# Kernel tuning notes

Hardware: AMD Instinct MI355X
Metric: run time of the kernel (lower is better)

The kernel has to match this reference:

```python
import jax, jax.numpy as jnp
import numpy as np

N0, N1, N2 = 100000, 50000, 20000
D = 128
E0, E1 = 600000, 300000


def _sage_rel(x_src, x_dst, src, dst, Ws, Wn, b, n_dst):
    """DGL SAGEConv(mean): fc_self(x_dst) + fc_neigh(mean of in-neighbors) + b."""
    msg = x_src[src]                                              # [E, D] gather
    ssum = jax.ops.segment_sum(msg, dst, num_segments=n_dst)      # [n_dst, D]
    deg = jax.ops.segment_sum(jnp.ones(dst.shape, x_src.dtype), dst, num_segments=n_dst)
    h_neigh = ssum / jnp.maximum(deg, 1.0)[:, None]               # zero-degree -> 0
    return x_dst @ Ws + h_neigh @ Wn + b


def setup_inputs() -> dict:
    key = jax.random.key(0)
    ks = jax.random.split(key, 24)
    p = 0.05
    inp = {
        "x": jax.random.normal(ks[0], (N0, D), jnp.float32),
        "e0_src_r0": jax.random.randint(ks[1], (E0,), 0, N0),
        "e0_dst_r0": jax.random.randint(ks[2], (E0,), 0, N1),
        "e0_src_r1": jax.random.randint(ks[3], (E0,), 0, N0),
        "e0_dst_r1": jax.random.randint(ks[4], (E0,), 0, N1),
        "e1_src_r0": jax.random.randint(ks[5], (E1,), 0, N1),
        "e1_dst_r0": jax.random.randint(ks[6], (E1,), 0, N2),
        "e1_src_r1": jax.random.randint(ks[7], (E1,), 0, N1),
        "e1_dst_r1": jax.random.randint(ks[8], (E1,), 0, N2),
    }
    names = ["Ws1_r0", "Wn1_r0", "Ws1_r1", "Wn1_r1", "Ws2_r0", "Wn2_r0", "Ws2_r1", "Wn2_r1"]
    for i, n in enumerate(names):
        inp[n] = jax.random.normal(ks[9 + i], (D, D), jnp.float32) * p
    for i, n in enumerate(["b1_r0", "b1_r1", "b2_r0", "b2_r1"]):
        inp[n] = jax.random.normal(ks[17 + i], (D,), jnp.float32) * p
    return inp


def reference(x, e0_src_r0, e0_dst_r0, e0_src_r1, e0_dst_r1,
              e1_src_r0, e1_dst_r0, e1_src_r1, e1_dst_r1,
              Ws1_r0, Wn1_r0, b1_r0, Ws1_r1, Wn1_r1, b1_r1,
              Ws2_r0, Wn2_r0, b2_r0, Ws2_r1, Wn2_r1, b2_r1):
    # Layer 1: HeteroGraphConv sum over relations, then ReLU
    x_dst1 = x[:N1]
    h1 = (_sage_rel(x, x_dst1, e0_src_r0, e0_dst_r0, Ws1_r0, Wn1_r0, b1_r0, N1)
          + _sage_rel(x, x_dst1, e0_src_r1, e0_dst_r1, Ws1_r1, Wn1_r1, b1_r1, N1))
    h1 = jax.nn.relu(h1)
    # Layer 2
    h1_dst = h1[:N2]
    h2 = (_sage_rel(h1, h1_dst, e1_src_r0, e1_dst_r0, Ws2_r0, Wn2_r0, b2_r0, N2)
          + _sage_rel(h1, h1_dst, e1_src_r1, e1_dst_r1, Ws2_r1, Wn2_r1, b2_r1, N2))
    return h2
```

## Files before the change

kernel.cpp:

```cpp
#include <hip/hip_runtime.h>
#include <hip/hip_bf16.h>
#include <hip/hip_fp8.h>

#define N0 100000
#define N1 50000
#define N2 20000
#define DD 128
#define E0 600000
#define E1 300000

#define NSEG_TOT (2 * N1 + 2 * N2)
#define ETOT     (2 * E0 + 2 * E1)

#define SEG_SHIFT 9
#define NBK  ((NSEG_TOT + 511) / 512)
#define CH   2048
#define NCH  ((ETOT + CH - 1) / CH)
#define PADCAP 8192

#define CAST_BLOCKS 6250
#define PREP_BLOCKS 48
#define PROLOGUE_BLOCKS (CAST_BLOCKS + PREP_BLOCKS + NCH)

typedef __attribute__((ext_vector_type(8))) short short8;
typedef __attribute__((ext_vector_type(4))) float floatx4;
typedef __attribute__((ext_vector_type(2))) float floatx2;

__device__ __forceinline__ void st2bf(__hip_bfloat16* p, float a, float b) {
    __hip_bfloat162 v;
    v.x = __float2bfloat16(a);
    v.y = __float2bfloat16(b);
    *(__hip_bfloat162*)p = v;
}
__device__ __forceinline__ short bf16bits(float v) {
    __hip_bfloat16 b = __float2bfloat16(v);
    return *(short*)&b;
}
__device__ __forceinline__ float bf2f(unsigned short u) {
    return __uint_as_float(((unsigned int)u) << 16);
}
__device__ __forceinline__ float4 ld4bf(const __hip_bfloat16* p) {
    ushort4 u = *(const ushort4*)p;
    return make_float4(bf2f(u.x), bf2f(u.y), bf2f(u.z), bf2f(u.w));
}
__device__ __forceinline__ void st4bf(__hip_bfloat16* p, float4 v) {
    short vs[4];
    vs[0] = bf16bits(v.x); vs[1] = bf16bits(v.y);
    vs[2] = bf16bits(v.z); vs[3] = bf16bits(v.w);
    *(int2*)p = *(int2*)vs;
}

__device__ __forceinline__ unsigned f8enc4(float x, float y, float z, float w) {
    int v = 0;
    v = __builtin_amdgcn_cvt_pk_fp8_f32(x, y, v, false);
    v = __builtin_amdgcn_cvt_pk_fp8_f32(z, w, v, true);
    return (unsigned)v;
}
__device__ __forceinline__ void f8acc8m(unsigned lo, unsigned hi, float m, float* acc) {
    floatx2 p0 = __builtin_amdgcn_cvt_pk_f32_fp8((int)lo, false);
    floatx2 p1 = __builtin_amdgcn_cvt_pk_f32_fp8((int)lo, true);
    floatx2 p2 = __builtin_amdgcn_cvt_pk_f32_fp8((int)hi, false);
    floatx2 p3 = __builtin_amdgcn_cvt_pk_f32_fp8((int)hi, true);
    acc[0] = fmaf(m, p0[0], acc[0]); acc[1] = fmaf(m, p0[1], acc[1]);
    acc[2] = fmaf(m, p1[0], acc[2]); acc[3] = fmaf(m, p1[1], acc[3]);
    acc[4] = fmaf(m, p2[0], acc[4]); acc[5] = fmaf(m, p2[1], acc[5]);
    acc[6] = fmaf(m, p3[0], acc[6]); acc[7] = fmaf(m, p3[1], acc[7]);
}

__device__ __forceinline__ int scan256(int s, int* sh, int t) {
    sh[t] = s;
    __syncthreads();
    for (int off = 1; off < 256; off <<= 1) {
        int tmp = (t >= off) ? sh[t - off] : 0;
        __syncthreads();
        sh[t] += tmp;
        __syncthreads();
    }
    return sh[t];
}

__device__ __forceinline__ int2 edge_seg_src(int e,
    const int* s0, const int* d0, const int* s1, const int* d1,
    const int* s2, const int* d2, const int* s3, const int* d3)
{
    if (e < E0)               return make_int2(s0[e],            d0[e]);
    if (e < 2 * E0)           return make_int2(s1[e - E0],       N1 + d1[e - E0]);
    if (e < 2 * E0 + E1)      return make_int2(s2[e - 2 * E0],   2 * N1 + d2[e - 2 * E0]);
    int ee = e - 2 * E0 - E1;
    return make_int2(s3[ee], 2 * N1 + N2 + d3[ee]);
}

__global__ __launch_bounds__(256) void prologue_kernel(
    const float* __restrict__ x, __hip_bfloat16* __restrict__ xb,
    unsigned char* __restrict__ xf8,
    const int* __restrict__ s0a, const int* __restrict__ d0a,
    const int* __restrict__ s0b, const int* __restrict__ d0b,
    const int* __restrict__ s1a, const int* __restrict__ d1a,
    const int* __restrict__ s1b, const int* __restrict__ d1b,
    int* __restrict__ cntmat, int* __restrict__ ofsmat,
    unsigned* __restrict__ chunkbuf,
    const float* __restrict__ Ws1a, const float* __restrict__ Ws1b,
    const float* __restrict__ Wn1a, const float* __restrict__ Wn1b,
    const float* __restrict__ Ws2a, const float* __restrict__ Ws2b,
    const float* __restrict__ Wn2a, const float* __restrict__ Wn2b,
    short* __restrict__ wfrag1, short* __restrict__ wfrag2)
{
    __shared__ int hist[512];
    __shared__ int ofs[512];
    __shared__ int sh[256];
    __shared__ unsigned rec[CH];
    const int bid = blockIdx.x;
    const int t = threadIdx.x;

    if (bid < CAST_BLOCKS) {
        int i = bid * 256 + t;
        const float4* xp = (const float4*)x + (size_t)i * 2;
        float4 a = xp[0], b = xp[1];
        __hip_bfloat16* pb = xb + (size_t)i * 8;
        st2bf(pb + 0, a.x, a.y); st2bf(pb + 2, a.z, a.w);
        st2bf(pb + 4, b.x, b.y); st2bf(pb + 6, b.z, b.w);
        uint2 w8;
        w8.x = f8enc4(a.x, a.y, a.z, a.w);
        w8.y = f8enc4(b.x, b.y, b.z, b.w);
        *(uint2*)(xf8 + (size_t)i * 8) = w8;
    } else if (bid < CAST_BLOCKS + PREP_BLOCKS) {
        int p = (bid - CAST_BLOCKS) * 256 + t;
        int layer = p >= 6144;
        int q = p - layer * 6144;
        int lane = q & 63;
        int mt = (q >> 6) & 7;
        int kc = q >> 9;
        int n = mt * 16 + (lane & 15);
        int k0 = kc * 32 + ((lane >> 4) << 3);
        const float* Wsa = layer ? Ws2a : Ws1a;
        const float* Wsb = layer ? Ws2b : Ws1b;
        const float* Wna = layer ? Wn2a : Wn1a;
        const float* Wnb = layer ? Wn2b : Wn1b;
        short* wf = layer ? wfrag2 : wfrag1;
        short vals[8];
#pragma unroll
        for (int j = 0; j < 8; j++) {
            int k = k0 + j;
            float w;
            if (k < 128)      w = Wsa[k * DD + n] + Wsb[k * DD + n];
            else if (k < 256) w = Wna[(k - 128) * DD + n];
            else              w = Wnb[(k - 256) * DD + n];
            vals[j] = bf16bits(w);
        }
        *(short8*)(wf + (size_t)q * 8) = *(short8*)vals;
    } else {
        const int chunk = bid - CAST_BLOCKS - PREP_BLOCKS;
        const int ebase = chunk * CH;
        const int ecount = (ETOT - ebase < CH) ? (ETOT - ebase) : CH;

        hist[t] = 0; hist[t + 256] = 0;
        __syncthreads();

        int2 myrec[CH / 256];
#pragma unroll
        for (int it = 0; it < CH / 256; it++) {
            int e = ebase + it * 256 + t;
            int2 r = make_int2(0, -1);
            if (e < ETOT) {
                r = edge_seg_src(e, s0a, d0a, s0b, d0b, s1a, d1a, s1b, d1b);
                atomicAdd(&hist[r.y >> SEG_SHIFT], 1);
            }
            myrec[it] = r;
        }
        __syncthreads();

        const int l0 = 2 * t, l1 = 2 * t + 1;
        int c0 = hist[l0], c1 = hist[l1];
        int s = c0 + c1;
        int incl = scan256(s, sh, t);
        int ex = incl - s;
        ofs[l0] = ex;
        ofs[l1] = ex + c0;
        __syncthreads();

        for (int g = t; g < NBK; g += 256) {
            cntmat[(size_t)g * NCH + chunk] = hist[g];
            ofsmat[(size_t)g * NCH + chunk] = ofs[g];
        }
        __syncthreads();

#pragma unroll
        for (int it = 0; it < CH / 256; it++) {
            int2 r = myrec[it];
            if (r.y >= 0) {
                int rk = atomicAdd(&ofs[r.y >> SEG_SHIFT], 1);
                rec[rk] = (unsigned)r.x | ((unsigned)(r.y & 511) << 17);
            }
        }
        __syncthreads();

        for (int i = t; i < ecount; i += 256)
            chunkbuf[ebase + i] = rec[i];
    }
}

__global__ __launch_bounds__(256) void csr_finalize_kernel(
    const unsigned* __restrict__ chunkbuf,
    const int* __restrict__ cntmat, const int* __restrict__ ofsmat,
    int* __restrict__ row_beg, int* __restrict__ row_cnt,
    int* __restrict__ eidx)
{
    __shared__ int sh[256];
    __shared__ int preL[NCH];
    __shared__ int lenL[NCH];
    __shared__ int cnt[512];
    __shared__ int excl[512];
    __shared__ unsigned rec[PADCAP];
    const int t = threadIdx.x;
    const int g = blockIdx.x;
    const int l0 = 2 * t, l1 = 2 * t + 1;

    int v[4]; int s = 0;
#pragma unroll
    for (int i = 0; i < 4; i++) {
        int idx = t * 4 + i;
        v[i] = (idx < NCH) ? cntmat[(size_t)g * NCH + idx] : 0;
        s += v[i];
    }
    int incl = scan256(s, sh, t);
    int ex = incl - s;
#pragma unroll
    for (int i = 0; i < 4; i++) {
        int idx = t * 4 + i;
        if (idx < NCH) { preL[idx] = ex; lenL[idx] = v[i]; }
        ex += v[i];
    }
    int Eloc = sh[255];
    if (Eloc > PADCAP) Eloc = PADCAP;
    cnt[l0] = 0; cnt[l1] = 0;
    __syncthreads();

    for (int c = t; c < NCH; c += 256) {
        int len = lenL[c];
        int dst = preL[c];
        int off = ofsmat[(size_t)g * NCH + c];
        const unsigned* src = chunkbuf + (size_t)c * CH + off;
        for (int i = 0; i < len; i++) rec[dst + i] = src[i];
    }
    __syncthreads();

    for (int i = t; i < Eloc; i += 256)
        atomicAdd(&cnt[rec[i] >> 17], 1);
    __syncthreads();

    int c0 = cnt[l0], c1 = cnt[l1];
    int ssum = c0 + c1;
    int inc2 = scan256(ssum, sh, t);
    int ex2 = inc2 - ssum;
    excl[l0] = ex2;
    excl[l1] = ex2 + c0;
    __syncthreads();

    const int segbase = g << SEG_SHIFT;
    const int base = g * PADCAP;
    int nloc = NSEG_TOT - segbase;
    if (nloc > 512) nloc = 512;
    for (int l = t; l < nloc; l += 256) {
        row_beg[segbase + l] = base + excl[l];
        row_cnt[segbase + l] = cnt[l];
    }
    __syncthreads();
    cnt[l0] = 0; cnt[l1] = 0;
    __syncthreads();

    for (int i = t; i < Eloc; i += 256) {
        unsigned r = rec[i];
        int l = r >> 17;
        int pos = atomicAdd(&cnt[l], 1);
        eidx[base + excl[l] + pos] = (int)(r & 0x1FFFF);
    }
}

__global__ __launch_bounds__(256) void aggregate_fp8_kernel(
    const unsigned char* __restrict__ xf8,
    const int* __restrict__ row_beg, const int* __restrict__ row_cnt,
    const int* __restrict__ eidx,
    __hip_bfloat16* __restrict__ hn,
    int nseg)
{
    int wid = (blockIdx.x * 256 + threadIdx.x) >> 6;
    const int lane = threadIdx.x & 63;
    if (wid >= nseg) return;
    wid = __builtin_amdgcn_readfirstlane(wid);

    const int beg = row_beg[wid];
    const int cnt = row_cnt[wid];
    const int end = beg + cnt;
    const int q = lane >> 4;
    const int l16 = lane & 15;

    float acc[8];
#pragma unroll
    for (int j = 0; j < 8; j++) acc[j] = 0.f;

    for (int kb = beg; kb < end; kb += 16) {
        int nrows = end - kb;
        if (nrows > 16) nrows = 16;
        int myidx = eidx[kb + (l16 < nrows ? l16 : nrows - 1)];
        uint2 vv[4];
        float mm[4];
#pragma unroll
        for (int j = 0; j < 4; j++) {
            int r = q + 4 * j;
            int sl = r < nrows ? r : nrows - 1;
            int ri = __shfl(myidx, sl);
            vv[j] = *(const uint2*)(xf8 + (size_t)ri * DD + l16 * 8);
            mm[j] = (r < nrows) ? 1.f : 0.f;
        }
#pragma unroll
        for (int j = 0; j < 4; j++)
            f8acc8m(vv[j].x, vv[j].y, mm[j], acc);
    }

#pragma unroll
    for (int j = 0; j < 8; j++) {
        acc[j] += __shfl_xor(acc[j], 16);
        acc[j] += __shfl_xor(acc[j], 32);
    }

    if (lane < 16) {
        const float inv = 1.f / (float)(cnt > 1 ? cnt : 1);
        short vs[8];
#pragma unroll
        for (int j = 0; j < 8; j++) vs[j] = bf16bits(acc[j] * inv);
        *(int4*)(hn + (size_t)wid * DD + l16 * 8) = *(int4*)vs;
    }
}

__global__ __launch_bounds__(256) void aggregate_kernel(
    const __hip_bfloat16* __restrict__ xb,
    const int* __restrict__ row_beg, const int* __restrict__ row_cnt,
    const int* __restrict__ eidx,
    __hip_bfloat16* __restrict__ hn,
    int nseg)
{
    int wid = (blockIdx.x * 256 + threadIdx.x) >> 6;
    const int lane = threadIdx.x & 63;
    if (wid >= nseg) return;
    wid = __builtin_amdgcn_readfirstlane(wid);

    const int beg = row_beg[wid];
    const int cnt = row_cnt[wid];
    const int end = beg + cnt;
    const int half = lane >> 5;
    const int l32 = lane & 31;

    float4 s = make_float4(0.f, 0.f, 0.f, 0.f);
    for (int kb = beg; kb < end; kb += 16) {
        int nrows = end - kb;
        if (nrows > 16) nrows = 16;
        int myidx = eidx[kb + (l32 < nrows ? l32 : nrows - 1)];
        ushort4 vv[8];
        float mm[8];
#pragma unroll
        for (int j = 0; j < 8; j++) {
            int r = half + 2 * j;
            int sl = r < nrows ? r : nrows - 1;
            int ri = __shfl(myidx, sl);
            vv[j] = *(const ushort4*)(xb + (long)ri * DD + l32 * 4);
            mm[j] = (r < nrows) ? 1.f : 0.f;
        }
#pragma unroll
        for (int j = 0; j < 8; j++) {
            s.x = fmaf(mm[j], bf2f(vv[j].x), s.x);
            s.y = fmaf(mm[j], bf2f(vv[j].y), s.y);
            s.z = fmaf(mm[j], bf2f(vv[j].z), s.z);
            s.w = fmaf(mm[j], bf2f(vv[j].w), s.w);
        }
    }

    s.x += __shfl_xor(s.x, 32);
    s.y += __shfl_xor(s.y, 32);
    s.z += __shfl_xor(s.z, 32);
    s.w += __shfl_xor(s.w, 32);

    if (!half) {
        const float inv = 1.f / (float)(cnt > 1 ? cnt : 1);
        float4 m = make_float4(s.x * inv, s.y * inv, s.z * inv, s.w * inv);
        st4bf(hn + (long)wid * DD + l32 * 4, m);
    }
}

template <bool RELU, typename TOUT>
__global__ __launch_bounds__(256) void mfma_combine_kernel(
    const __hip_bfloat16* __restrict__ xself,
    const __hip_bfloat16* __restrict__ hn,
    const short* __restrict__ wfrag,
    const float* __restrict__ b0, const float* __restrict__ b1,
    TOUT* __restrict__ out, int M)
{
    const int t = threadIdx.x;
    const int wave = t >> 6;
    const int lane = t & 63;
    const int nsub = lane & 15;
    const int quad = lane >> 4;
    const int base = blockIdx.x * 128 + wave * 32;

    const int node0 = base + nsub;
    const int node1 = base + 16 + nsub;
    const long n0c = node0 < M ? node0 : M - 1;
    const long n1c = node1 < M ? node1 : M - 1;

    floatx4 acc[2][8];
#pragma unroll
    for (int nt = 0; nt < 2; nt++)
#pragma unroll
        for (int mt = 0; mt < 8; mt++) acc[nt][mt] = (floatx4){0.f, 0.f, 0.f, 0.f};

    for (int kc = 0; kc < 12; kc++) {
        const __hip_bfloat16* src;
        long r0, r1;
        int koff;
        if (kc < 4)      { src = xself; koff = kc * 32;       r0 = n0c;     r1 = n1c; }
        else if (kc < 8) { src = hn;    koff = (kc - 4) * 32; r0 = n0c;     r1 = n1c; }
        else             { src = hn;    koff = (kc - 8) * 32; r0 = M + n0c; r1 = M + n1c; }

        short8 bf0 = *(const short8*)(src + r0 * DD + koff + quad * 8);
        short8 bf1 = *(const short8*)(src + r1 * DD + koff + quad * 8);
        const short* wbase = wfrag + ((size_t)(kc * 8) * 64 + lane) * 8;
#pragma unroll
        for (int mt = 0; mt < 8; mt++) {
            short8 af = *(const short8*)(wbase + (size_t)mt * 64 * 8);
            acc[0][mt] = __builtin_amdgcn_mfma_f32_16x16x32_bf16(af, bf0, acc[0][mt], 0, 0, 0);
            acc[1][mt] = __builtin_amdgcn_mfma_f32_16x16x32_bf16(af, bf1, acc[1][mt], 0, 0, 0);
        }
    }

#pragma unroll
    for (int nt = 0; nt < 2; nt++) {
        int node = (nt == 0) ? node0 : node1;
        if (node >= M) continue;
#pragma unroll
        for (int mt = 0; mt < 8; mt++) {
            int c0 = mt * 16 + quad * 4;
            float4 bb0 = *(const float4*)(b0 + c0);
            float4 bb1 = *(const float4*)(b1 + c0);
            float v0 = acc[nt][mt][0] + bb0.x + bb1.x;
            float v1 = acc[nt][mt][1] + bb0.y + bb1.y;
            float v2 = acc[nt][mt][2] + bb0.z + bb1.z;
            float v3 = acc[nt][mt][3] + bb0.w + bb1.w;
            if (RELU) {
                v0 = v0 > 0.f ? v0 : 0.f;
                v1 = v1 > 0.f ? v1 : 0.f;
                v2 = v2 > 0.f ? v2 : 0.f;
                v3 = v3 > 0.f ? v3 : 0.f;
            }
            TOUT* p = out + (long)node * DD + c0;
            if constexpr (sizeof(TOUT) == 4) {
                *(float4*)p = make_float4(v0, v1, v2, v3);
            } else {
                short vs[4];
                vs[0] = bf16bits(v0); vs[1] = bf16bits(v1);
                vs[2] = bf16bits(v2); vs[3] = bf16bits(v3);
                *(int2*)p = *(int2*)vs;
            }
        }
    }
}


extern "C" void kernel_launch(void* const* d_in, const int* in_sizes, int n_in,
                              void* d_out, int out_size, void* d_ws, size_t ws_size,
                              hipStream_t stream)
{
    const float* x = (const float*)d_in[0];
    const int* e0_src_r0 = (const int*)d_in[1];
    const int* e0_dst_r0 = (const int*)d_in[2];
    const int* e0_src_r1 = (const int*)d_in[3];
    const int* e0_dst_r1 = (const int*)d_in[4];
    const int* e1_src_r0 = (const int*)d_in[5];
    const int* e1_dst_r0 = (const int*)d_in[6];
    const int* e1_src_r1 = (const int*)d_in[7];
    const int* e1_dst_r1 = (const int*)d_in[8];
    const float* Ws1_r0 = (const float*)d_in[9];
    const float* Wn1_r0 = (const float*)d_in[10];
    const float* Ws1_r1 = (const float*)d_in[11];
    const float* Wn1_r1 = (const float*)d_in[12];
    const float* Ws2_r0 = (const float*)d_in[13];
    const float* Wn2_r0 = (const float*)d_in[14];
    const float* Ws2_r1 = (const float*)d_in[15];
    const float* Wn2_r1 = (const float*)d_in[16];
    const float* b1_r0 = (const float*)d_in[17];
    const float* b1_r1 = (const float*)d_in[18];
    const float* b2_r0 = (const float*)d_in[19];
    const float* b2_r1 = (const float*)d_in[20];
    float* out = (float*)d_out;

    __hip_bfloat16* xb = (__hip_bfloat16*)d_ws;
    __hip_bfloat16* h1 = xb;
    unsigned char* xf8 = (unsigned char*)(xb + (size_t)N0 * DD);
    __hip_bfloat16* hn = (__hip_bfloat16*)(xf8 + (size_t)N0 * DD);
    unsigned* chunkbuf = (unsigned*)hn;
    int* eidx     = (int*)(hn + (size_t)2 * N1 * DD);
    int* row_beg  = eidx + NBK * PADCAP;
    int* row_cnt  = row_beg + NSEG_TOT;
    int* cntmat   = row_cnt + NSEG_TOT;
    int* ofsmat   = cntmat + NBK * NCH;
    short* wfrag1 = (short*)(ofsmat + NBK * NCH);
    short* wfrag2 = wfrag1 + 12 * 8 * 64 * 8;

    prologue_kernel<<<PROLOGUE_BLOCKS, 256, 0, stream>>>(
        x, xb, xf8,
        e0_src_r0, e0_dst_r0, e0_src_r1, e0_dst_r1,
        e1_src_r0, e1_dst_r0, e1_src_r1, e1_dst_r1,
        cntmat, ofsmat, chunkbuf,
        Ws1_r0, Ws1_r1, Wn1_r0, Wn1_r1,
        Ws2_r0, Ws2_r1, Wn2_r0, Wn2_r1,
        wfrag1, wfrag2);

    csr_finalize_kernel<<<NBK, 256, 0, stream>>>(
        chunkbuf, cntmat, ofsmat, row_beg, row_cnt, eidx);

    aggregate_fp8_kernel<<<(2 * N1 + 3) / 4, 256, 0, stream>>>(
        xf8, row_beg, row_cnt, eidx, hn, 2 * N1);
    mfma_combine_kernel<true, __hip_bfloat16>
        <<<(N1 + 127) / 128, 256, 0, stream>>>(xb, hn, wfrag1, b1_r0, b1_r1, h1, N1);

    aggregate_kernel<<<(2 * N2 + 3) / 4, 256, 0, stream>>>(
        h1, row_beg + 2 * N1, row_cnt + 2 * N1, eidx, hn, 2 * N2);
    mfma_combine_kernel<false, float>
        <<<(N2 + 127) / 128, 256, 0, stream>>>(h1, hn, wfrag2, b2_r0, b2_r1, out, N2);
}
```

Baseline: 266.0 us.

## Process four segments per wavefront in both aggregation kernels

Both aggregation kernels now assign one 16-lane quarter of a wavefront to each destination segment instead of one full wavefront per segment. This removes the cross-lane reductions and idle lanes that came from spreading a short segment (about 6 edges on average) over 64 lanes, and it cuts the grid size by four. Each quarter loops up to the maximum count among its four segments and masks the extra iterations, so segments with uneven degree leave some lanes idle. Launch counts are computed as 2*N/16, which depends on the node counts dividing evenly.

Result: faster. 258.2 us, median of 2 (-2.9%).

```diff
diff --git a/kernel.cpp b/kernel.cpp
--- a/kernel.cpp
+++ b/kernel.cpp
@@ -283,53 +283,52 @@
     __hip_bfloat16* __restrict__ hn,
     int nseg)
 {
-    int wid = (blockIdx.x * 256 + threadIdx.x) >> 6;
+    const int wv = (blockIdx.x * 256 + threadIdx.x) >> 6;
     const int lane = threadIdx.x & 63;
-    if (wid >= nseg) return;
-    wid = __builtin_amdgcn_readfirstlane(wid);
-
-    const int beg = row_beg[wid];
-    const int cnt = row_cnt[wid];
-    const int end = beg + cnt;
-    const int q = lane >> 4;
     const int l16 = lane & 15;
+    const int seg = wv * 4 + (lane >> 4);
+    if (seg >= nseg) return;
+
+    const int beg = row_beg[seg];
+    const int cnt = row_cnt[seg];
+
+    int mc = cnt;
+    mc = max(mc, __shfl_xor(mc, 16));
+    mc = max(mc, __shfl_xor(mc, 32));
+    mc = __builtin_amdgcn_readfirstlane(mc);
 
     float acc[8];
 #pragma unroll
     for (int j = 0; j < 8; j++) acc[j] = 0.f;
 
-    for (int kb = beg; kb < end; kb += 16) {
-        int nrows = end - kb;
-        if (nrows > 16) nrows = 16;
-        int myidx = eidx[kb + (l16 < nrows ? l16 : nrows - 1)];
-        uint2 vv[4];
-        float mm[4];
-#pragma unroll
-        for (int j = 0; j < 4; j++) {
-            int r = q + 4 * j;
-            int sl = r < nrows ? r : nrows - 1;
-            int ri = __shfl(myidx, sl);
-            vv[j] = *(const uint2*)(xf8 + (size_t)ri * DD + l16 * 8);
-            mm[j] = (r < nrows) ? 1.f : 0.f;
-        }
-#pragma unroll
-        for (int j = 0; j < 4; j++)
-            f8acc8m(vv[j].x, vv[j].y, mm[j], acc);
-    }
-
-#pragma unroll
-    for (int j = 0; j < 8; j++) {
-        acc[j] += __shfl_xor(acc[j], 16);
-        acc[j] += __shfl_xor(acc[j], 32);
-    }
-
-    if (lane < 16) {
-        const float inv = 1.f / (float)(cnt > 1 ? cnt : 1);
-        short vs[8];
-#pragma unroll
-        for (int j = 0; j < 8; j++) vs[j] = bf16bits(acc[j] * inv);
-        *(int4*)(hn + (size_t)wid * DD + l16 * 8) = *(int4*)vs;
-    }
+    for (int kb = 0; kb < mc; kb += 16) {
+        int ii = kb + l16;
+        int safe = (cnt > 0) ? (ii < cnt ? ii : cnt - 1) : 0;
+        int myidx = eidx[beg + safe];
+#pragma unroll
+        for (int h = 0; h < 2; h++) {
+            int rb = kb + h * 8;
+            if (rb >= mc) break;
+            uint2 vv[8];
+#pragma unroll
+            for (int j = 0; j < 8; j++) {
+                int ri = __shfl(myidx, (lane & 48) | (h * 8 + j));
+                ri = (rb + j < cnt) ? ri : 0;
+                vv[j] = *(const uint2*)(xf8 + (size_t)ri * DD + l16 * 8);
+            }
+#pragma unroll
+            for (int j = 0; j < 8; j++) {
+                float m = (rb + j < cnt) ? 1.f : 0.f;
+                f8acc8m(vv[j].x, vv[j].y, m, acc);
+            }
+        }
+    }
+
+    const float inv = 1.f / (float)(cnt > 1 ? cnt : 1);
+    short vs[8];
+#pragma unroll
+    for (int j = 0; j < 8; j++) vs[j] = bf16bits(acc[j] * inv);
+    *(int4*)(hn + (size_t)seg * DD + l16 * 8) = *(int4*)vs;
 }
 
 __global__ __launch_bounds__(256) void aggregate_kernel(
@@ -339,51 +338,61 @@
     __hip_bfloat16* __restrict__ hn,
     int nseg)
 {
-    int wid = (blockIdx.x * 256 + threadIdx.x) >> 6;
+    const int wv = (blockIdx.x * 256 + threadIdx.x) >> 6;
     const int lane = threadIdx.x & 63;
-    if (wid >= nseg) return;
-    wid = __builtin_amdgcn_readfirstlane(wid);
-
-    const int beg = row_beg[wid];
-    const int cnt = row_cnt[wid];
-    const int end = beg + cnt;
-    const int half = lane >> 5;
-    const int l32 = lane & 31;
-
-    float4 s = make_float4(0.f, 0.f, 0.f, 0.f);
-    for (int kb = beg; kb < end; kb += 16) {
-        int nrows = end - kb;
-        if (nrows > 16) nrows = 16;
-        int myidx = eidx[kb + (l32 < nrows ? l32 : nrows - 1)];
-        ushort4 vv[8];
-        float mm[8];
-#pragma unroll
-        for (int j = 0; j < 8; j++) {
-            int r = half + 2 * j;
-            int sl = r < nrows ? r : nrows - 1;
-            int ri = __shfl(myidx, sl);
-            vv[j] = *(const ushort4*)(xb + (long)ri * DD + l32 * 4);
-            mm[j] = (r < nrows) ? 1.f : 0.f;
-        }
-#pragma unroll
-        for (int j = 0; j < 8; j++) {
-            s.x = fmaf(mm[j], bf2f(vv[j].x), s.x);
-            s.y = fmaf(mm[j], bf2f(vv[j].y), s.y);
-            s.z = fmaf(mm[j], bf2f(vv[j].z), s.z);
-            s.w = fmaf(mm[j], bf2f(vv[j].w), s.w);
-        }
-    }
-
-    s.x += __shfl_xor(s.x, 32);
-    s.y += __shfl_xor(s.y, 32);
-    s.z += __shfl_xor(s.z, 32);
-    s.w += __shfl_xor(s.w, 32);
-
-    if (!half) {
-        const float inv = 1.f / (float)(cnt > 1 ? cnt : 1);
-        float4 m = make_float4(s.x * inv, s.y * inv, s.z * inv, s.w * inv);
-        st4bf(hn + (long)wid * DD + l32 * 4, m);
-    }
+    const int l16 = lane & 15;
+    const int seg = wv * 4 + (lane >> 4);
+    if (seg >= nseg) return;
+
+    const int beg = row_beg[seg];
+    const int cnt = row_cnt[seg];
+
+    int mc = cnt;
+    mc = max(mc, __shfl_xor(mc, 16));
+    mc = max(mc, __shfl_xor(mc, 32));
+    mc = __builtin_amdgcn_readfirstlane(mc);
+
+    float acc[8];
+#pragma unroll
+    for (int j = 0; j < 8; j++) acc[j] = 0.f;
+
+    for (int kb = 0; kb < mc; kb += 16) {
+        int ii = kb + l16;
+        int safe = (cnt > 0) ? (ii < cnt ? ii : cnt - 1) : 0;
+        int myidx = eidx[beg + safe];
+#pragma unroll
+        for (int h = 0; h < 2; h++) {
+            int rb = kb + h * 8;
+            if (rb >= mc) break;
+            ushort4 va[8], vb[8];
+#pragma unroll
+            for (int j = 0; j < 8; j++) {
+                int ri = __shfl(myidx, (lane & 48) | (h * 8 + j));
+                ri = (rb + j < cnt) ? ri : 0;
+                const __hip_bfloat16* p = xb + (long)ri * DD + l16 * 8;
+                va[j] = *(const ushort4*)p;
+                vb[j] = *(const ushort4*)(p + 4);
+            }
+#pragma unroll
+            for (int j = 0; j < 8; j++) {
+                float m = (rb + j < cnt) ? 1.f : 0.f;
+                acc[0] = fmaf(m, bf2f(va[j].x), acc[0]);
+                acc[1] = fmaf(m, bf2f(va[j].y), acc[1]);
+                acc[2] = fmaf(m, bf2f(va[j].z), acc[2]);
+                acc[3] = fmaf(m, bf2f(va[j].w), acc[3]);
+                acc[4] = fmaf(m, bf2f(vb[j].x), acc[4]);
+                acc[5] = fmaf(m, bf2f(vb[j].y), acc[5]);
+                acc[6] = fmaf(m, bf2f(vb[j].z), acc[6]);
+                acc[7] = fmaf(m, bf2f(vb[j].w), acc[7]);
+            }
+        }
+    }
+
+    const float inv = 1.f / (float)(cnt > 1 ? cnt : 1);
+    short vs[8];
+#pragma unroll
+    for (int j = 0; j < 8; j++) vs[j] = bf16bits(acc[j] * inv);
+    *(int4*)(hn + (size_t)seg * DD + l16 * 8) = *(int4*)vs;
 }
 
 template <bool RELU, typename TOUT>
@@ -516,12 +525,12 @@
     csr_finalize_kernel<<<NBK, 256, 0, stream>>>(
         chunkbuf, cntmat, ofsmat, row_beg, row_cnt, eidx);
 
-    aggregate_fp8_kernel<<<(2 * N1 + 3) / 4, 256, 0, stream>>>(
+    aggregate_fp8_kernel<<<(2 * N1) / 16, 256, 0, stream>>>(
         xf8, row_beg, row_cnt, eidx, hn, 2 * N1);
     mfma_combine_kernel<true, __hip_bfloat16>
         <<<(N1 + 127) / 128, 256, 0, stream>>>(xb, hn, wfrag1, b1_r0, b1_r1, h1, N1);
 
-    aggregate_kernel<<<(2 * N2 + 3) / 4, 256, 0, stream>>>(
+    aggregate_kernel<<<(2 * N2) / 16, 256, 0, stream>>>(
         h1, row_beg + 2 * N1, row_cnt + 2 * N1, eidx, hn, 2 * N2);
     mfma_combine_kernel<false, float>
         <<<(N2 + 127) / 128, 256, 0, stream>>>(h1, hn, wfrag2, b2_r0, b2_r1, out, N2);
```
